# Kernel tuning notes

Measured on AMD Instinct MI355X. Metric: run time of the kernel, lower is better.

## Reference

```python
import jax, jax.numpy as jnp
import numpy as np
from jax import lax

LEVEL = 128  # level_num

def _bn(x, g, b, m, v):
    # inference-mode BatchNorm, channel axis = 1
    sh = (1, -1) + (1,) * (x.ndim - 2)
    return (x - m.reshape(sh)) * (g.reshape(sh) * lax.rsqrt(v.reshape(sh) + 1e-5)) + b.reshape(sh)

def _leaky(a):
    return jnp.where(a > 0, a, 0.01 * a)

def _l2n(a):
    return a / jnp.maximum(jnp.linalg.norm(a, axis=1, keepdims=True), 1e-12)

def _resize_bilinear_ac(x, oh, ow):
    # bilinear, align_corners=True, NCHW
    n, c, h, w = x.shape
    ys = jnp.linspace(0.0, h - 1.0, oh)
    xs = jnp.linspace(0.0, w - 1.0, ow)
    y0 = jnp.floor(ys).astype(jnp.int32)
    x0 = jnp.floor(xs).astype(jnp.int32)
    y1 = jnp.minimum(y0 + 1, h - 1)
    x1 = jnp.minimum(x0 + 1, w - 1)
    wy = (ys - y0)[:, None]
    wx = (xs - x0)[None, :]
    Y0, Y1, X0, X1 = y0[:, None], y1[:, None], x0[None, :], x1[None, :]
    return (x[:, :, Y0, X0] * (1 - wy) * (1 - wx) + x[:, :, Y0, X1] * (1 - wy) * wx
            + x[:, :, Y1, X0] * wy * (1 - wx) + x[:, :, Y1, X1] * wy * wx)

def _forward(x, conv1_w, bn1_g, bn1_b, bn1_m, bn1_v, conv2_w, f1_w, f2_w, f2_g, f2_b, f2_m, f2_v,
             out1_w, out1_g, out1_b, out1_m, out1_v, k_w, q_w, v_w, out_w, out_g, out_b, out_m, out_v):
    # conv1: 3x3 conv + BN + LeakyReLU
    y = lax.conv_general_dilated(x, conv1_w, (1, 1), 'SAME', dimension_numbers=('NCHW', 'OIHW', 'NCHW'))
    y = _leaky(_bn(y, bn1_g, bn1_b, bn1_m, bn1_v))
    # conv2: 1x1 conv, 256->128
    x2 = jnp.einsum('nchw,oc->nohw', y, conv2_w)
    N, C, H, W = x2.shape  # C = 128
    x_ave = x2.mean(axis=(2, 3), keepdims=True)  # [N,C,1,1]
    cos = (_l2n(x_ave) * _l2n(x2)).sum(1)        # [N,H,W]
    sh, sw = H // 3, W // 3
    L = sh * sw
    # H,W divisible by 3 -> adaptive_avg_pool2d is identity
    cs = cos.reshape(N, 3, sh, 3, sw).transpose(0, 1, 3, 2, 4).reshape(N, 9, L).transpose(0, 2, 1)  # [N,L,9]
    # LBP bit packing vs center (index 4); weight 0 at index 4 (strict > gives 0 there)
    bits = (cs > cs[:, :, 4:5]).astype(x.dtype)
    wts = jnp.array([1, 2, 4, 8, 0, 16, 32, 64, 128], dtype=x.dtype)
    code = (bits * wts).sum(-1)  # [N,L]
    mn = code.min(-1, keepdims=True)
    mx = code.max(-1, keepdims=True)
    code = (code - mn) / (mx - mn)
    cmin = code.min(-1, keepdims=True)
    cmax = code.max(-1, keepdims=True)
    qlv = (2 * jnp.arange(LEVEL, dtype=x.dtype) + 1) / (2 * LEVEL) * (cmax - cmin) + cmin  # [N,LEVEL]
    inter = (qlv[:, 1] - qlv[:, 0])[:, None, None]  # [N,1,1]
    quant = 1 - jnp.abs(qlv[:, None, :] - code[:, :, None])  # [N,L,LEVEL]
    quant = jnp.where(quant > 1 - inter, quant, 0.0)
    sta = quant.sum(1)                                       # [N,LEVEL]
    sta = sta / sta.sum(-1, keepdims=True)
    sta2 = jnp.stack([qlv, sta], axis=1)                     # [N,2,LEVEL]
    h1 = _leaky(jnp.einsum('ncl,oc->nol', sta2, f1_w))       # f1: 2->64
    h2 = jax.nn.relu(_bn(jnp.einsum('ncl,oc->nol', h1, f2_w), f2_g, f2_b, f2_m, f2_v))  # f2: 64->128
    xa = jnp.broadcast_to(x_ave[:, :, 0, 0][:, :, None], (N, C, LEVEL))
    s = jnp.concatenate([h2, xa], axis=1)                    # [N,256,LEVEL]
    s = jax.nn.relu(_bn(jnp.einsum('ncl,oc->nol', s, out1_w), out1_g, out1_b, out1_m, out1_v))
    k = jnp.einsum('ncl,oc->nol', s, k_w)
    q = jnp.einsum('ncl,oc->nol', s, q_w)
    v = jnp.einsum('ncl,oc->nol', s, v_w)
    w = jax.nn.softmax(jnp.einsum('ncl,ncm->nlm', k, q), axis=-1)  # bmm(k^T, q)
    f = jnp.einsum('nlm,ncm->ncl', w, v)                            # bmm(w, v^T) then transpose
    f = jax.nn.relu(_bn(jnp.einsum('ncl,oc->nol', f, out_w), out_g, out_b, out_m, out_v))
    out = jnp.einsum('ncl,npl->ncp', f, quant).reshape(N, 256, sh, sh)  # bmm(f, quant^T)
    return _resize_bilinear_ac(out, H, W)

def setup_inputs() -> dict:
    key = jax.random.key(0)
    ks = jax.random.split(key, 16)
    f32 = jnp.float32
    def nrm(k, shape, s=0.05):
        return s * jax.random.normal(k, shape, f32)
    def bnp(k, c):
        k1, k2, k3, k4 = jax.random.split(k, 4)
        return (1.0 + 0.1 * jax.random.normal(k1, (c,), f32),
                0.1 * jax.random.normal(k2, (c,), f32),
                0.1 * jax.random.normal(k3, (c,), f32),
                jax.random.uniform(k4, (c,), f32, 0.5, 1.5))
    d = {}
    d['x'] = jax.random.normal(ks[0], (32, 512, 48, 48), f32)
    d['conv1_w'] = nrm(ks[1], (256, 512, 3, 3))
    d['bn1_g'], d['bn1_b'], d['bn1_m'], d['bn1_v'] = bnp(ks[2], 256)
    d['conv2_w'] = nrm(ks[3], (128, 256))
    d['f1_w'] = nrm(ks[4], (64, 2), 0.3)
    d['f2_w'] = nrm(ks[5], (128, 64), 0.1)
    d['f2_g'], d['f2_b'], d['f2_m'], d['f2_v'] = bnp(ks[6], 128)
    d['out1_w'] = nrm(ks[7], (256, 256))
    d['out1_g'], d['out1_b'], d['out1_m'], d['out1_v'] = bnp(ks[8], 256)
    d['k_w'] = nrm(ks[9], (256, 256))
    d['q_w'] = nrm(ks[10], (256, 256))
    d['v_w'] = nrm(ks[11], (256, 256))
    d['out_w'] = nrm(ks[12], (256, 256))
    d['out_g'], d['out_b'], d['out_m'], d['out_v'] = bnp(ks[13], 256)
    return d

def reference(x, conv1_w, bn1_g, bn1_b, bn1_m, bn1_v, conv2_w, f1_w, f2_w, f2_g, f2_b, f2_m, f2_v,
              out1_w, out1_g, out1_b, out1_m, out1_v, k_w, q_w, v_w, out_w, out_g, out_b, out_m, out_v):
    return _forward(x, conv1_w, bn1_g, bn1_b, bn1_m, bn1_v, conv2_w, f1_w, f2_w, f2_g, f2_b, f2_m, f2_v,
                    out1_w, out1_g, out1_b, out1_m, out1_v, k_w, q_w, v_w, out_w, out_g, out_b, out_m, out_v)
```

## Files before the change

### kernel.cpp

```cpp
#include <hip/hip_runtime.h>
#include <math.h>

#define N_IMG 32
#define P2304 2304
#define CIN 512
#define CMID 256
#define C2 128
#define LEV 128

typedef _Float16 half8 __attribute__((ext_vector_type(8)));
typedef float f32x16 __attribute__((ext_vector_type(16)));
typedef unsigned short u16;
typedef unsigned int u32;

__device__ __forceinline__ float wredSum(float v){
#pragma unroll
  for (int o = 32; o > 0; o >>= 1) v += __shfl_down(v, o, 64);
  return v;
}
__device__ __forceinline__ float wredMax(float v){
#pragma unroll
  for (int o = 32; o > 0; o >>= 1) v = fmaxf(v, __shfl_down(v, o, 64));
  return v;
}
__device__ __forceinline__ float wredMin(float v){
#pragma unroll
  for (int o = 32; o > 0; o >>= 1) v = fminf(v, __shfl_down(v, o, 64));
  return v;
}

__device__ __forceinline__ void gll16(const void* g, void* l){
  __builtin_amdgcn_global_load_lds(
      (const __attribute__((address_space(1))) void*)g,
      (__attribute__((address_space(3))) void*)l, 16, 0, 0);
}

__global__ void prep_w1_kernel(const float* __restrict__ w1,
                               uint4* __restrict__ Wh, uint4* __restrict__ Wl){
  int fid = blockIdx.x * 256 + threadIdx.x;
  int lam = fid & 63;
  int c32 = (fid >> 6) & 3;
  int cot = (fid >> 8) & 1;
  int kt  = fid >> 9;
  int co = cot * 128 + c32 * 32 + (lam & 31);
  half8 vh, vl;
#pragma unroll
  for (int j = 0; j < 8; ++j){
    int k = kt * 16 + ((lam >> 5) << 3) + j;
    int r = k >> 9;
    int ci = k & 511;
    float v = w1[co * (CIN * 9) + ci * 9 + r];
    _Float16 h = (_Float16)v;
    vh[j] = h;
    vl[j] = (_Float16)((v - (float)h) * 2048.0f);
  }
  Wh[fid] = *(uint4*)&vh;
  Wl[fid] = *(uint4*)&vl;
}

__global__ void prep_w2_kernel(const float* __restrict__ w2,
                               uint4* __restrict__ Wh, uint4* __restrict__ Wl){
  int fid = blockIdx.x * 256 + threadIdx.x;
  int lam = fid & 63;
  int c32 = (fid >> 6) & 3;
  int kt  = fid >> 8;
  int co = c32 * 32 + (lam & 31);
  half8 vh, vl;
#pragma unroll
  for (int j = 0; j < 8; ++j){
    int k = kt * 16 + ((lam >> 5) << 3) + j;
    float v = w2[co * CMID + k];
    _Float16 h = (_Float16)v;
    vh[j] = h;
    vl[j] = (_Float16)((v - (float)h) * 2048.0f);
  }
  Wh[fid] = *(uint4*)&vh;
  Wl[fid] = *(uint4*)&vl;
}

__global__ void prep_bn_kernel(const float* __restrict__ g1, const float* __restrict__ b1,
                               const float* __restrict__ m1, const float* __restrict__ v1,
                               float* __restrict__ s1, float* __restrict__ t1){
  int c = threadIdx.x;
  float s = g1[c] * (1.0f / sqrtf(v1[c] + 1e-5f));
  s1[c] = s;
  t1[c] = b1[c] - m1[c] * s;
}

__global__ void prep_x_kernel(const float* __restrict__ x,
                              u16* __restrict__ xh, u16* __restrict__ xl,
                              int n0){
  __shared__ float tile[128 * 49];
  const int t = threadIdx.x;
  const int b = blockIdx.x;
  const int n_loc = b / 50;
  const int hp = b - n_loc * 50;
  const int n = n0 + n_loc;
  const int h = hp - 1;
  const bool vrow = (h >= 0) && (h < 48);
  const size_t base_n = (size_t)n_loc * 1280000;
  for (int cc = 0; cc < 4; ++cc){
    if (vrow){
      const float* src = x + (((size_t)n * 512 + cc * 128) * 48 + h) * 48;
#pragma unroll
      for (int i = 0; i < 24; ++i){
        int idx = t + 256 * i;
        int w = idx % 48;
        int c = idx / 48;
        tile[c * 49 + w] = src[(size_t)c * 2304 + w];
      }
    }
    __syncthreads();
    for (int i = 0; i < 13; ++i){
      int idx = t + 256 * i;
      if (idx < 3200){
        int ck_loc = idx / 400;
        int rem = idx - ck_loc * 400;
        int wp = rem >> 3;
        int clp = rem & 7;
        int w = wp - 1;
        int c_loc = ck_loc * 16 + clp * 2;
        float v0 = 0.f, v1 = 0.f;
        if (vrow && (unsigned)w < 48u){
          v0 = tile[c_loc * 49 + w];
          v1 = tile[(c_loc + 1) * 49 + w];
        }
        _Float16 h0 = (_Float16)v0, h1 = (_Float16)v1;
        _Float16 l0 = (_Float16)((v0 - (float)h0) * 2048.0f);
        _Float16 l1 = (_Float16)((v1 - (float)h1) * 2048.0f);
        union { _Float16 hh[2]; u32 uu; } ph, pl;
        ph.hh[0] = h0; ph.hh[1] = h1;
        pl.hh[0] = l0; pl.hh[1] = l1;
        size_t off = base_n + ((size_t)(cc * 8 + ck_loc) * 2500
                               + hp * 50 + wp) * 16 + clp * 2;
        *(u32*)(xh + off) = ph.uu;
        *(u32*)(xl + off) = pl.uu;
      }
    }
    __syncthreads();
  }
}

#define COMPUTE_M(CUR, KF)                                                    \
  {                                                                           \
    const int ct0 = (g & 1) * 2, pt0 = (g >> 1) * 2;                          \
    half8 fAh[2], fAl[2], fBh[2], fBl[2];                                     \
    _Pragma("unroll")                                                         \
    for (int a = 0; a < 2; ++a){                                              \
      fAh[a] = *(half8*)&Abuf[CUR][KF][0][(ct0 + a) * 512 + lam * 8];         \
      fAl[a] = *(half8*)&Abuf[CUR][KF][1][(ct0 + a) * 512 + lam * 8];         \
      fBh[a] = *(half8*)&Bbuf[CUR][KF][0][(pt0 + a) * 512 + lam * 8];         \
      fBl[a] = *(half8*)&Bbuf[CUR][KF][1][(pt0 + a) * 512 + lam * 8];         \
    }                                                                         \
    _Pragma("unroll")                                                         \
    for (int a = 0; a < 2; ++a)                                               \
      _Pragma("unroll")                                                       \
      for (int b = 0; b < 2; ++b){                                            \
        acc_hh[a][b] = __builtin_amdgcn_mfma_f32_32x32x16_f16(                \
            fAh[a], fBh[b], acc_hh[a][b], 0, 0, 0);                           \
        acc_x[a][b] = __builtin_amdgcn_mfma_f32_32x32x16_f16(                 \
            fAh[a], fBl[b], acc_x[a][b], 0, 0, 0);                            \
        acc_x[a][b] = __builtin_amdgcn_mfma_f32_32x32x16_f16(                 \
            fAl[a], fBh[b], acc_x[a][b], 0, 0, 0);                            \
      }                                                                       \
  }

#define WAITV8  asm volatile("s_waitcnt vmcnt(8)"  ::: "memory")
#define WAITV0  asm volatile("s_waitcnt vmcnt(0)"  ::: "memory")
#define BARSB { __builtin_amdgcn_s_barrier(); __builtin_amdgcn_sched_barrier(0); }

template<int NC>
__global__ __launch_bounds__(256, 2) void conv1_lds_kernel(
    const u16* __restrict__ xh, const u16* __restrict__ xl,
    const uint4* __restrict__ Wh, const uint4* __restrict__ Wl,
    const float* __restrict__ s1, const float* __restrict__ t1,
    u16* __restrict__ yh, u16* __restrict__ yl, int n0)
{
  __shared__ _Float16 Abuf[2][2][2][2048];
  __shared__ _Float16 Bbuf[2][2][2][2048];
  const int t = threadIdx.x;
  const int lam = t & 63;
  const int g = t >> 6;

  const int xcd = blockIdx.x & 7;
  const int rest = blockIdx.x >> 3;
  const int NPX = NC / 8;
  const int n_loc = xcd * NPX + rest / 36;
  const int inner = rest % 36;
  const int pt_blk = inner % 18;
  const int cot = inner / 18;
  const int n = n0 + n_loc;

  const int pbase = pt_blk * 128;
  const int khi = lam >> 5;
  const int pp = (g << 5) + (lam & 31);
  const int p = pbase + pp;
  const int ph = p / 48, pw = p - ph * 48;
  const u16* xh_n = xh + (size_t)n_loc * 1280000;
  const u16* xl_n = xl + (size_t)n_loc * 1280000;

  const int S = 144;

  f32x16 acc_hh[2][2], acc_x[2][2];
#pragma unroll
  for (int a = 0; a < 2; ++a)
#pragma unroll
    for (int b = 0; b < 2; ++b){
#pragma unroll
      for (int e = 0; e < 16; ++e){ acc_hh[a][b][e] = 0.f; acc_x[a][b][e] = 0.f; }
    }

#define ISSUE1(SV, BUF)                                                       \
  {                                                                           \
    int s_ = (SV);                                                            \
    int k0_ = 2 * s_;                                                         \
    _Pragma("unroll")                                                         \
    for (int kf = 0; kf < 2; ++kf){                                           \
      int fg_ = ((k0_ + kf) * 2 + cot) * 4 + g;                               \
      gll16(Wh + fg_ * 64 + lam, &Abuf[BUF][kf][0][t * 8]);                   \
      gll16(Wl + fg_ * 64 + lam, &Abuf[BUF][kf][1][t * 8]);                   \
    }                                                                         \
    int r_ = k0_ >> 5;                                          \
    int ck0_ = k0_ & 31;                         \
    int qpp_ = (ph + r_ / 3) * 50 + (pw + r_ % 3);            \
    _Pragma("unroll")                                                         \
    for (int kf = 0; kf < 2; ++kf){                                           \
      size_t o_ = ((size_t)(ck0_ + kf) * 2500 + qpp_) * 16 + (khi << 3);      \
      gll16(xh_n + o_, &Bbuf[BUF][kf][0][t * 8]);                             \
      gll16(xl_n + o_, &Bbuf[BUF][kf][1][t * 8]);                             \
    }                                                                         \
  }

  ISSUE1(0, 0);
  ISSUE1(1, 1);

  for (int s = 0; s < S - 1; ++s){
    WAITV8;
    BARSB;
    __builtin_amdgcn_s_setprio(1);
    COMPUTE_M(s & 1, 0);
    COMPUTE_M(s & 1, 1);
    __builtin_amdgcn_s_setprio(0);
    if (s + 2 < S){
      BARSB;
      ISSUE1(s + 2, s & 1);
    }
  }
  WAITV0;
  BARSB;
  __builtin_amdgcn_s_setprio(1);
  COMPUTE_M((S - 1) & 1, 0);
  COMPUTE_M((S - 1) & 1, 1);
  __builtin_amdgcn_s_setprio(0);
#undef ISSUE1

  const int cobase = cot * 128;
#pragma unroll
  for (int a = 0; a < 2; ++a){
    const int ctile = (g & 1) * 2 + a;
#pragma unroll
    for (int b = 0; b < 2; ++b){
      const int ptile = (g >> 1) * 2 + b;
      const int pg = pbase + ptile * 32 + (lam & 31);
#pragma unroll
      for (int q = 0; q < 4; ++q){
        const int co0 = cobase + ctile * 32 + 8 * q + 4 * khi;
        const int co16 = co0 >> 4, col = co0 & 15;
        union { _Float16 h[4]; uint2 u; } Uh, Ul;
#pragma unroll
        for (int i = 0; i < 4; ++i){
          const int rg = 4 * q + i;
          const int co = co0 + i;
          float val = acc_hh[a][b][rg] + acc_x[a][b][rg] * (1.0f / 2048.0f);
          val = val * s1[co] + t1[co];
          val = val > 0.f ? val : 0.01f * val;
          _Float16 h = (_Float16)val;
          Uh.h[i] = h;
          Ul.h[i] = (_Float16)((val - (float)h) * 2048.0f);
        }
        size_t off = (((size_t)n * 16 + co16) * P2304 + pg) * 16 + col;
        *(uint2*)(yh + off) = Uh.u;
        *(uint2*)(yl + off) = Ul.u;
      }
    }
  }
}

__global__ __launch_bounds__(256, 2) void conv2_lds_kernel(
    const u16* __restrict__ yh, const u16* __restrict__ yl,
    const uint4* __restrict__ Wh, const uint4* __restrict__ Wl,
    float* __restrict__ out)
{
  __shared__ _Float16 Abuf[2][2][2][2048];
  __shared__ _Float16 Bbuf[2][2][2][2048];
  const int t = threadIdx.x;
  const int lam = t & 63;
  const int g = t >> 6;

  const int pt_blk = blockIdx.x % 18;
  const int n = blockIdx.x / 18;
  const int pbase = pt_blk * 128;
  const int khi = lam >> 5;
  const int p = pbase + (g << 5) + (lam & 31);
  const u16* yh_n = yh + (size_t)n * 589824;
  const u16* yl_n = yl + (size_t)n * 589824;

  const int S = 8;

  f32x16 acc_hh[2][2], acc_x[2][2];
#pragma unroll
  for (int a = 0; a < 2; ++a)
#pragma unroll
    for (int b = 0; b < 2; ++b){
#pragma unroll
      for (int e = 0; e < 16; ++e){ acc_hh[a][b][e] = 0.f; acc_x[a][b][e] = 0.f; }
    }

#define ISSUE2(SV, BUF)                                                       \
  {                                                                           \
    int s_ = (SV);                                                            \
    int k0_ = 2 * s_;                                                         \
    _Pragma("unroll")                                                         \
    for (int kf = 0; kf < 2; ++kf){                                           \
      int fg_ = (k0_ + kf) * 4 + g;                                           \
      gll16(Wh + fg_ * 64 + lam, &Abuf[BUF][kf][0][t * 8]);                   \
      gll16(Wl + fg_ * 64 + lam, &Abuf[BUF][kf][1][t * 8]);                   \
    }                                                                         \
    _Pragma("unroll")                                                         \
    for (int kf = 0; kf < 2; ++kf){                                           \
      size_t o_ = ((size_t)(k0_ + kf) * P2304 + p) * 16 + (khi << 3);         \
      gll16(yh_n + o_, &Bbuf[BUF][kf][0][t * 8]);                             \
      gll16(yl_n + o_, &Bbuf[BUF][kf][1][t * 8]);                             \
    }                                                                         \
  }

  ISSUE2(0, 0);
  ISSUE2(1, 1);

  for (int s = 0; s < S - 1; ++s){
    WAITV8;
    BARSB;
    __builtin_amdgcn_s_setprio(1);
    COMPUTE_M(s & 1, 0);
    COMPUTE_M(s & 1, 1);
    __builtin_amdgcn_s_setprio(0);
    if (s + 2 < S){
      BARSB;
      ISSUE2(s + 2, s & 1);
    }
  }
  WAITV0;
  BARSB;
  __builtin_amdgcn_s_setprio(1);
  COMPUTE_M((S - 1) & 1, 0);
  COMPUTE_M((S - 1) & 1, 1);
  __builtin_amdgcn_s_setprio(0);
#undef ISSUE2

#pragma unroll
  for (int a = 0; a < 2; ++a){
    const int ctile = (g & 1) * 2 + a;
#pragma unroll
    for (int b = 0; b < 2; ++b){
      const int ptile = (g >> 1) * 2 + b;
      const int pg = pbase + ptile * 32 + (lam & 31);
#pragma unroll
      for (int rg = 0; rg < 16; ++rg){
        const int row = (rg & 3) + 8 * (rg >> 2) + 4 * khi;
        const int co = ctile * 32 + row;
        float val = acc_hh[a][b][rg] + acc_x[a][b][rg] * (1.0f / 2048.0f);
        out[((size_t)n * C2 + co) * P2304 + pg] = val;
      }
    }
  }
}

template<int R, int CPT, int COTN, bool BN>
__global__ __launch_bounds__(256, 2) void conv_mfma_kernel(
    const float* __restrict__ in, const uint4* __restrict__ Wh, const uint4* __restrict__ Wl,
    const float* __restrict__ s1, const float* __restrict__ t1, float* __restrict__ out)
{
  __shared__ _Float16 Abuf[2][2][2][2048];
  __shared__ _Float16 Bbuf[2][2][2][2048];
  const int t = threadIdx.x;
  const int lam = t & 63;
  const int g = t >> 6;

  int n, pt_blk, cot;
  if (COTN == 2){
    int xcd = blockIdx.x & 7;
    int rest = blockIdx.x >> 3;
    n = xcd * 4 + rest / 36;
    int inner = rest % 36;
    pt_blk = inner % 18;
    cot = inner / 18;
  } else {
    pt_blk = blockIdx.x % 18;
    cot = 0;
    n = blockIdx.x / 18;
  }
  const int pbase = pt_blk * 128;
  const int cobase = cot * 128;

  const int khi = lam >> 5;
  const int pp = (g << 5) + (lam & 31);
  const int p = pbase + pp;
  const int ph = p / 48, pw = p - ph * 48;
  const float* in_n = in + (size_t)n * CPT * P2304;

  const int S = (R * CPT) / 32;
  const int KTPT = CPT / 16;

  f32x16 acc_hh[2][2], acc_x[2][2];
#pragma unroll
  for (int a = 0; a < 2; ++a)
#pragma unroll
    for (int b = 0; b < 2; ++b){
#pragma unroll
      for (int e = 0; e < 16; ++e){ acc_hh[a][b][e] = 0.f; acc_x[a][b][e] = 0.f; }
    }

  uint4 rAh[2], rAl[2];
  float rB[16];
  bool vmask;

#define ISSUE(SV)                                                             \
  {                                                                           \
    int s_ = (SV);                                                            \
    _Pragma("unroll")                                                         \
    for (int kf = 0; kf < 2; ++kf){                                           \
      int fi = (((2 * s_ + kf) * COTN + cot) * 4 + g) * 64 + lam;             \
      rAh[kf] = Wh[fi];                                                       \
      rAl[kf] = Wl[fi];                                                       \
    }                                                                         \
    int r_ = (R == 1) ? 0 : ((2 * s_) / KTPT);                                \
    int cbase_ = ((2 * s_) % KTPT) * 16;                                      \
    int dh_ = (R == 1) ? 0 : (r_ / 3 - 1);                                    \
    int dw_ = (R == 1) ? 0 : (r_ - (r_ / 3) * 3 - 1);                         \
    int hh_ = ph + dh_, ww_ = pw + dw_;                                       \
    vmask = ((unsigned)hh_ < 48u) & ((unsigned)ww_ < 48u);                    \
    int hc_ = min(max(hh_, 0), 47), wc_ = min(max(ww_, 0), 47);               \
    const float* src_ = in_n + hc_ * 48 + wc_                                 \
                        + (size_t)(cbase_ + khi * 8) * P2304;                 \
    _Pragma("unroll")                                                         \
    for (int kf = 0; kf < 2; ++kf)                                            \
      _Pragma("unroll")                                                       \
      for (int j = 0; j < 8; ++j)                                             \
        rB[kf * 8 + j] = src_[(kf * 16 + j) * P2304];                         \
  }

#define STASH(NXT)                                                            \
  {                                                                           \
    _Pragma("unroll")                                                         \
    for (int kf = 0; kf < 2; ++kf){                                           \
      *(uint4*)&Abuf[NXT][kf][0][t * 8] = rAh[kf];                            \
      *(uint4*)&Abuf[NXT][kf][1][t * 8] = rAl[kf];                            \
      half8 vh, vl;                                                           \
      _Pragma("unroll")                                                       \
      for (int j = 0; j < 8; ++j){                                            \
        float v = vmask ? rB[kf * 8 + j] : 0.0f;                              \
        _Float16 h = (_Float16)v;                                             \
        vh[j] = h;                                                            \
        vl[j] = (_Float16)((v - (float)h) * 2048.0f);                         \
      }                                                                       \
      *(half8*)&Bbuf[NXT][kf][0][t * 8] = vh;                                 \
      *(half8*)&Bbuf[NXT][kf][1][t * 8] = vl;                                 \
    }                                                                         \
  }

  ISSUE(0);
  STASH(0);
  __syncthreads();

  for (int s = 0; s < S; ++s){
    const int cur = s & 1, nxt = cur ^ 1;
    const bool more = (s + 1 < S);
    if (more) ISSUE(s + 1);
    COMPUTE_M(cur, 0);
    if (more) STASH(nxt);
    COMPUTE_M(cur, 1);
    __syncthreads();
  }
#undef ISSUE
#undef STASH

  const int M = COTN * 128;
#pragma unroll
  for (int a = 0; a < 2; ++a){
    const int ctile = (g & 1) * 2 + a;
#pragma unroll
    for (int b = 0; b < 2; ++b){
      const int ptile = (g >> 1) * 2 + b;
      const int pg = pbase + ptile * 32 + (lam & 31);
#pragma unroll
      for (int rg = 0; rg < 16; ++rg){
        const int row = (rg & 3) + 8 * (rg >> 2) + 4 * (lam >> 5);
        const int co = cobase + ctile * 32 + row;
        float val = acc_hh[a][b][rg] + acc_x[a][b][rg] * (1.0f / 2048.0f);
        if (BN){
          val = val * s1[co] + t1[co];
          val = val > 0.f ? val : 0.01f * val;
        }
        out[((size_t)n * M + co) * P2304 + pg] = val;
      }
    }
  }
}

__global__ void xave_kernel(const float* __restrict__ x2, float* __restrict__ xave){
  __shared__ float red[4];
  int nc = blockIdx.x, t = threadIdx.x;
  const float* row = x2 + nc * P2304;
  float s = 0.f;
#pragma unroll
  for (int i = 0; i < 9; i++) s += row[t + 256 * i];
  float w = wredSum(s);
  if ((t & 63) == 0) red[t >> 6] = w;
  __syncthreads();
  if (t == 0) xave[nc] = (red[0] + red[1] + red[2] + red[3]) * (1.0f / 2304.0f);
}

__global__ void xan_kernel(const float* __restrict__ xave, float* __restrict__ xan){
  __shared__ float red[2];
  int n = blockIdx.x, t = threadIdx.x;
  float v = xave[n * 128 + t];
  float w = wredSum(v * v);
  if ((t & 63) == 0) red[t >> 6] = w;
  __syncthreads();
  float norm = fmaxf(sqrtf(red[0] + red[1]), 1e-12f);
  xan[n * 128 + t] = v / norm;
}

__global__ void cos_kernel(const float* __restrict__ x2, const float* __restrict__ xan,
                           float* __restrict__ cosb){
  int idx = blockIdx.x * 256 + threadIdx.x;
  if (idx >= N_IMG * P2304) return;
  int n = idx / P2304;
  int p = idx - n * P2304;
  const float* xp = x2 + n * C2 * P2304 + p;
  const float* an = xan + n * 128;
  float dot = 0.f, ss = 0.f;
  for (int c = 0; c < 128; c++){
    float v = xp[c * P2304];
    dot += an[c] * v;
    ss  += v * v;
  }
  cosb[idx] = dot / fmaxf(sqrtf(ss), 1e-12f);
}

__global__ void lbp_kernel(const float* __restrict__ cosb, float* __restrict__ code,
                           float* __restrict__ qlv){
  __shared__ float red[4];
  int n = blockIdx.x;
  int l = threadIdx.x;
  int ir = l >> 4, ic = l & 15;
  const float* cn = cosb + n * P2304;
  float cs4 = cn[(16 + ir) * 48 + (16 + ic)];
  const float wts[9] = {1.f, 2.f, 4.f, 8.f, 0.f, 16.f, 32.f, 64.f, 128.f};
  float codev = 0.f;
#pragma unroll
  for (int j = 0; j < 9; j++){
    int jr = j / 3, jc = j - 3 * (j / 3);
    float vv = cn[(jr * 16 + ir) * 48 + (jc * 16 + ic)];
    if (vv > cs4) codev += wts[j];
  }
  float w;
  w = wredMin(codev);
  if ((l & 63) == 0) red[l >> 6] = w;
  __syncthreads();
  float mn = fminf(fminf(red[0], red[1]), fminf(red[2], red[3]));
  __syncthreads();
  w = wredMax(codev);
  if ((l & 63) == 0) red[l >> 6] = w;
  __syncthreads();
  float mx = fmaxf(fmaxf(red[0], red[1]), fmaxf(red[2], red[3]));
  __syncthreads();
  float cd = (codev - mn) / (mx - mn);
  w = wredMin(cd);
  if ((l & 63) == 0) red[l >> 6] = w;
  __syncthreads();
  float cmin = fminf(fminf(red[0], red[1]), fminf(red[2], red[3]));
  __syncthreads();
  w = wredMax(cd);
  if ((l & 63) == 0) red[l >> 6] = w;
  __syncthreads();
  float cmax = fmaxf(fmaxf(red[0], red[1]), fmaxf(red[2], red[3]));
  code[n * 256 + l] = cd;
  if (l < 128){
    float tmp = (float)(2 * l + 1) * (1.0f / 256.0f);
    qlv[n * 128 + l] = tmp * (cmax - cmin) + cmin;
  }
}

__global__ void quant_kernel(const float* __restrict__ code, const float* __restrict__ qlv,
                             float* __restrict__ quantT){
  __shared__ float cs[256];
  __shared__ float qs[128];
  int n = blockIdx.x, t = threadIdx.x;
  cs[t] = code[n * 256 + t];
  if (t < 128) qs[t] = qlv[n * 128 + t];
  __syncthreads();
  float thr = 1.0f - (qs[1] - qs[0]);
  float* dst = quantT + n * LEV * 256;
#pragma unroll 4
  for (int i = 0; i < 128; i++){
    int v = t + 256 * i;
    int lv = v >> 8;
    int p = v & 255;
    float qq = 1.0f - fabsf(qs[lv] - cs[p]);
    dst[v] = (qq > thr) ? qq : 0.f;
  }
}

__global__ void sta_rows_kernel(const float* __restrict__ quantT, float* __restrict__ raw){
  int b = blockIdx.x;
  int t = threadIdx.x;
  int n = b >> 5;
  int row = (b & 31) * 4 + (t >> 6);
  int lane = t & 63;
  const float* src = quantT + ((size_t)(n * LEV + row)) * 256 + lane * 4;
  float4 v = *(const float4*)src;
  float s = v.x + v.y + v.z + v.w;
  s = wredSum(s);
  if (lane == 0) raw[n * 128 + row] = s;
}

__global__ void sta_norm_kernel(const float* __restrict__ raw, float* __restrict__ sta){
  __shared__ float red[2];
  int n = blockIdx.x, t = threadIdx.x;
  float v = raw[n * 128 + t];
  float w = wredSum(v);
  if ((t & 63) == 0) red[t >> 6] = w;
  __syncthreads();
  sta[n * 128 + t] = v / (red[0] + red[1]);
}

__global__ void h2_fused_kernel(const float* __restrict__ f1w, const float* __restrict__ f2w,
                                const float* __restrict__ qlv, const float* __restrict__ sta,
                                const float* __restrict__ g, const float* __restrict__ bb,
                                const float* __restrict__ mm, const float* __restrict__ vv,
                                float* __restrict__ h2){
  int idx = blockIdx.x * 256 + threadIdx.x;
  if (idx >= N_IMG * 32 * 128) return;
  int l = idx & 127;
  int o0 = ((idx >> 7) & 31) << 2;
  int n = idx >> 12;
  float qv = qlv[n * 128 + l];
  float sv = sta[n * 128 + l];
  const float* w0 = f2w + (o0 + 0) * 64;
  const float* w1 = f2w + (o0 + 1) * 64;
  const float* w2 = f2w + (o0 + 2) * 64;
  const float* w3 = f2w + (o0 + 3) * 64;
  float a0 = 0, a1 = 0, a2 = 0, a3 = 0;
  for (int c = 0; c < 64; c++){
    float hv = f1w[2 * c] * qv + f1w[2 * c + 1] * sv;
    hv = hv > 0.f ? hv : 0.01f * hv;
    a0 += w0[c] * hv; a1 += w1[c] * hv; a2 += w2[c] * hv; a3 += w3[c] * hv;
  }
  float av[4] = {a0, a1, a2, a3};
#pragma unroll
  for (int j = 0; j < 4; j++){
    int o = o0 + j;
    float s = g[o] * (1.0f / sqrtf(vv[o] + 1e-5f));
    float val = (av[j] - mm[o]) * s + bb[o];
    h2[(n * 128 + o) * 128 + l] = fmaxf(val, 0.f);
  }
}

__global__ void out1_fused_kernel(const float* __restrict__ Wm, const float* __restrict__ h2,
                                  const float* __restrict__ xave,
                                  const float* __restrict__ g, const float* __restrict__ bb,
                                  const float* __restrict__ mm, const float* __restrict__ vv,
                                  float* __restrict__ s2){
  int idx = blockIdx.x * 256 + threadIdx.x;
  if (idx >= N_IMG * 64 * 128) return;
  int l = idx & 127;
  int o0 = ((idx >> 7) & 63) << 2;
  int n = idx >> 13;
  const float* h2n = h2 + (n * 128) * 128 + l;
  const float* xa = xave + n * 128;
  const float* w0 = Wm + (o0 + 0) * 256;
  const float* w1 = Wm + (o0 + 1) * 256;
  const float* w2 = Wm + (o0 + 2) * 256;
  const float* w3 = Wm + (o0 + 3) * 256;
  float a0 = 0, a1 = 0, a2 = 0, a3 = 0;
  for (int c = 0; c < 128; c++){
    float bv = h2n[c * 128];
    a0 += w0[c] * bv; a1 += w1[c] * bv; a2 += w2[c] * bv; a3 += w3[c] * bv;
  }
  for (int c = 0; c < 128; c++){
    float bv = xa[c];
    a0 += w0[128 + c] * bv; a1 += w1[128 + c] * bv;
    a2 += w2[128 + c] * bv; a3 += w3[128 + c] * bv;
  }
  float av[4] = {a0, a1, a2, a3};
#pragma unroll
  for (int j = 0; j < 4; j++){
    int o = o0 + j;
    float s = g[o] * (1.0f / sqrtf(vv[o] + 1e-5f));
    float val = (av[j] - mm[o]) * s + bb[o];
    s2[(n * 256 + o) * 128 + l] = fmaxf(val, 0.f);
  }
}

__global__ void gemm_w_kernel(const float* __restrict__ Wm, const float* __restrict__ B,
                              float* __restrict__ Cout, int Cdim, int O, int total, int mode,
                              const float* __restrict__ g, const float* __restrict__ bb,
                              const float* __restrict__ mm, const float* __restrict__ vv){
  int idx = blockIdx.x * 256 + threadIdx.x;
  if (idx >= total) return;
  int per_n = (O >> 2) << 7;
  int n = idx / per_n;
  int rem = idx - n * per_n;
  int o0 = (rem >> 7) << 2;
  int l = rem & 127;
  const float* Bn = B + (n * Cdim) * 128 + l;
  const float* w0 = Wm + (o0 + 0) * Cdim;
  const float* w1 = Wm + (o0 + 1) * Cdim;
  const float* w2 = Wm + (o0 + 2) * Cdim;
  const float* w3 = Wm + (o0 + 3) * Cdim;
  float a0 = 0, a1 = 0, a2 = 0, a3 = 0;
  for (int c = 0; c < Cdim; c++){
    float bv = Bn[c * 128];
    a0 += w0[c] * bv; a1 += w1[c] * bv; a2 += w2[c] * bv; a3 += w3[c] * bv;
  }
  float av[4] = {a0, a1, a2, a3};
#pragma unroll
  for (int j = 0; j < 4; j++){
    int o = o0 + j;
    float val = av[j];
    if (mode == 1){
      float s = g[o] * (1.0f / sqrtf(vv[o] + 1e-5f));
      val = (val - mm[o]) * s + bb[o];
      val = fmaxf(val, 0.f);
    }
    Cout[(n * O + o) * 128 + l] = val;
  }
}

__global__ void gemm_kqv_kernel(const float* __restrict__ kW, const float* __restrict__ qW,
                                const float* __restrict__ vW, const float* __restrict__ B,
                                float* __restrict__ kO, float* __restrict__ qO,
                                float* __restrict__ vO){
  int idx = blockIdx.x * 256 + threadIdx.x;
  int sel = idx >> 18;
  int rem = idx & 262143;
  const float* Wm = (sel == 0) ? kW : (sel == 1) ? qW : vW;
  float* Cout     = (sel == 0) ? kO : (sel == 1) ? qO : vO;
  int n = rem >> 13;
  int r2 = rem & 8191;
  int o0 = (r2 >> 7) << 2;
  int l = r2 & 127;
  const float* Bn = B + (n * 256) * 128 + l;
  const float* w0 = Wm + (o0 + 0) * 256;
  const float* w1 = Wm + (o0 + 1) * 256;
  const float* w2 = Wm + (o0 + 2) * 256;
  const float* w3 = Wm + (o0 + 3) * 256;
  float a0 = 0, a1 = 0, a2 = 0, a3 = 0;
  for (int c = 0; c < 256; c++){
    float bv = Bn[c * 128];
    a0 += w0[c] * bv; a1 += w1[c] * bv; a2 += w2[c] * bv; a3 += w3[c] * bv;
  }
  float* dst = Cout + (n * 256 + o0) * 128 + l;
  dst[0] = a0; dst[128] = a1; dst[256] = a2; dst[384] = a3;
}

__global__ void attn_scsm_kernel(const float* __restrict__ k, const float* __restrict__ q,
                                 float* __restrict__ scT){
  __shared__ float redm[2][2][4];
  __shared__ float reds[2][2][4];
  int b = blockIdx.x;
  int t = threadIdx.x;
  int n = b >> 4;
  int h = t >> 7;
  int wv = (t >> 6) & 1;
  int lane = t & 63;
  int m = t & 127;
  int l0 = (((b & 15) * 2 + h)) * 4;
  const float* kn = k + n * 256 * 128;
  const float* qn = q + n * 256 * 128 + m;
  float a0 = 0, a1 = 0, a2 = 0, a3 = 0;
  for (int c = 0; c < 256; c++){
    float qv = qn[c * 128];
    const float* kr = kn + c * 128 + l0;
    a0 += kr[0] * qv; a1 += kr[1] * qv; a2 += kr[2] * qv; a3 += kr[3] * qv;
  }
  float av[4] = {a0, a1, a2, a3};
#pragma unroll
  for (int r = 0; r < 4; r++){
    float w = wredMax(av[r]);
    if (lane == 0) redm[h][wv][r] = w;
  }
  __syncthreads();
  float ex[4];
#pragma unroll
  for (int r = 0; r < 4; r++){
    float mx = fmaxf(redm[h][0][r], redm[h][1][r]);
    ex[r] = expf(av[r] - mx);
    float s = wredSum(ex[r]);
    if (lane == 0) reds[h][wv][r] = s;
  }
  __syncthreads();
  float* dst = scT + n * 16384 + m * 128 + l0;
#pragma unroll
  for (int r = 0; r < 4; r++){
    dst[r] = ex[r] / (reds[h][0][r] + reds[h][1][r]);
  }
}

__global__ void attn_f_kernel(const float* __restrict__ vb, const float* __restrict__ scT,
                              float* __restrict__ f){
  int idx = blockIdx.x * 256 + threadIdx.x;
  if (idx >= N_IMG * 64 * 128) return;
  int l = idx & 127;
  int c0 = ((idx >> 7) & 63) << 2;
  int n = idx >> 13;
  const float* vn = vb + (n * 256 + c0) * 128;
  const float* sn = scT + n * 128 * 128 + l;
  float a0 = 0, a1 = 0, a2 = 0, a3 = 0;
  for (int m = 0; m < 128; m++){
    float sv = sn[m * 128];
    a0 += vn[m] * sv; a1 += vn[128 + m] * sv; a2 += vn[256 + m] * sv; a3 += vn[384 + m] * sv;
  }
  float* dst = f + (n * 256 + c0) * 128 + l;
  dst[0] = a0; dst[128] = a1; dst[256] = a2; dst[384] = a3;
}

__global__ void final_kernel(const float* __restrict__ g, const float* __restrict__ quantT,
                             float* __restrict__ outs){
  int idx = blockIdx.x * 256 + threadIdx.x;
  if (idx >= N_IMG * 64 * 256) return;
  int p = idx & 255;
  int c0 = ((idx >> 8) & 63) << 2;
  int n = idx >> 14;
  const float* gn = g + (n * 256 + c0) * 128;
  const float* qn = quantT + (n * LEV) * 256 + p;
  float a0 = 0, a1 = 0, a2 = 0, a3 = 0;
  for (int lv = 0; lv < 128; lv++){
    float qv = qn[lv * 256];
    a0 += gn[lv] * qv; a1 += gn[128 + lv] * qv; a2 += gn[256 + lv] * qv; a3 += gn[384 + lv] * qv;
  }
  float* dst = outs + (n * 256 + c0) * 256 + p;
  dst[0] = a0; dst[256] = a1; dst[512] = a2; dst[768] = a3;
}

__global__ void resize_kernel(const float* __restrict__ outs, float* __restrict__ dout){
  int idx = blockIdx.x * 256 + threadIdx.x;
  if (idx >= N_IMG * 256 * P2304) return;
  int ow = idx % 48;
  int tmp = idx / 48;
  int oh = tmp % 48;
  int nc = tmp / 48;
  const float* src = outs + nc * 256;
  float fy = oh * (15.0f / 47.0f);
  float fx = ow * (15.0f / 47.0f);
  int y0 = (int)fy;
  int x0 = (int)fx;
  int y1 = min(y0 + 1, 15);
  int x1 = min(x0 + 1, 15);
  float wy = fy - (float)y0;
  float wx = fx - (float)x0;
  float v00 = src[y0 * 16 + x0], v01 = src[y0 * 16 + x1];
  float v10 = src[y1 * 16 + x0], v11 = src[y1 * 16 + x1];
  dout[idx] = v00 * (1.f - wy) * (1.f - wx) + v01 * (1.f - wy) * wx
            + v10 * wy * (1.f - wx) + v11 * wy * wx;
}

extern "C" void kernel_launch(void* const* d_in, const int* in_sizes, int n_in,
                              void* d_out, int out_size, void* d_ws, size_t ws_size,
                              hipStream_t stream)
{
  const float* x       = (const float*)d_in[0];
  const float* conv1_w = (const float*)d_in[1];
  const float* bn1_g   = (const float*)d_in[2];
  const float* bn1_b   = (const float*)d_in[3];
  const float* bn1_m   = (const float*)d_in[4];
  const float* bn1_v   = (const float*)d_in[5];
  const float* conv2_w = (const float*)d_in[6];
  const float* f1_w    = (const float*)d_in[7];
  const float* f2_w    = (const float*)d_in[8];
  const float* f2_g    = (const float*)d_in[9];
  const float* f2_b    = (const float*)d_in[10];
  const float* f2_m    = (const float*)d_in[11];
  const float* f2_v    = (const float*)d_in[12];
  const float* out1_w  = (const float*)d_in[13];
  const float* out1_g  = (const float*)d_in[14];
  const float* out1_b  = (const float*)d_in[15];
  const float* out1_m  = (const float*)d_in[16];
  const float* out1_v  = (const float*)d_in[17];
  const float* k_w     = (const float*)d_in[18];
  const float* q_w     = (const float*)d_in[19];
  const float* v_w     = (const float*)d_in[20];
  const float* out_w   = (const float*)d_in[21];
  const float* out_g   = (const float*)d_in[22];
  const float* out_b   = (const float*)d_in[23];
  const float* out_m   = (const float*)d_in[24];
  const float* out_v   = (const float*)d_in[25];

  float* ws = (float*)d_ws;
  float* dout = (float*)d_out;

  float* w_y   = ws;
  float* w_x2  = ws + 18874368;
  float* w_W1h = ws + 28311552;
  float* w_W1l = ws + 28901376;
  float* w_W2h = ws + 29491200;
  float* w_W2l = ws + 29507584;
  float* w_s1  = ws + 29523968;
  float* w_t1  = ws + 29524224;
  float* w_xave = w_y + 0;
  float* w_xan  = w_y + 4096;
  float* w_cos  = w_y + 8192;
  float* w_code = w_y + 81920;
  float* w_qlv  = w_y + 90112;
  float* w_sta  = w_y + 94208;
  float* w_quant= w_y + 98304;
  float* w_h2   = w_y + 1409024;
  float* w_k    = w_y + 2981888;
  float* w_q    = w_y + 4030464;
  float* w_v    = w_y + 5079040;
  float* w_scT  = w_y + 6651904;
  float* w_f    = w_y + 7176192;
  float* w_g    = w_y + 8224768;
  float* w_outs = w_y + 9273344;
  float* w_s2   = w_y + 11370496;
  float* w_raw  = w_y + 12419072;

  prep_w1_kernel<<<576, 256, 0, stream>>>(conv1_w, (uint4*)w_W1h, (uint4*)w_W1l);
  prep_w2_kernel<<<16, 256, 0, stream>>>(conv2_w, (uint4*)w_W2h, (uint4*)w_W2l);
  prep_bn_kernel<<<1, 256, 0, stream>>>(bn1_g, bn1_b, bn1_m, bn1_v, w_s1, w_t1);

  const size_t BASE_F = 29524480;
  const size_t XPI_F  = 640000;
  const size_t ws_f = ws_size / 4;
  int NCc = 0;
  if (ws_f >= BASE_F + 2 * 32 * XPI_F)      NCc = 32;
  else if (ws_f >= BASE_F + 2 * 16 * XPI_F) NCc = 16;

  if (NCc > 0){
    u16* w_xh = (u16*)(ws + BASE_F);
    u16* w_xl = w_xh + (size_t)NCc * 1280000;
    u16* w_yh = (u16*)w_y;
    u16* w_yl = (u16*)(w_y + 9437184);
    const int nchunk = N_IMG / NCc;
    for (int c = 0; c < nchunk; ++c){
      int n0 = c * NCc;
      prep_x_kernel<<<NCc * 50, 256, 0, stream>>>(x, w_xh, w_xl, n0);
      if (NCc == 32)
        conv1_lds_kernel<32><<<1152, 256, 0, stream>>>(
            w_xh, w_xl, (const uint4*)w_W1h, (const uint4*)w_W1l, w_s1, w_t1,
            w_yh, w_yl, n0);
      else
        conv1_lds_kernel<16><<<576, 256, 0, stream>>>(
            w_xh, w_xl, (const uint4*)w_W1h, (const uint4*)w_W1l, w_s1, w_t1,
            w_yh, w_yl, n0);
    }
    conv2_lds_kernel<<<576, 256, 0, stream>>>(
        w_yh, w_yl, (const uint4*)w_W2h, (const uint4*)w_W2l, w_x2);
  } else {
    conv_mfma_kernel<9, 512, 2, true><<<1152, 256, 0, stream>>>(
        x, (const uint4*)w_W1h, (const uint4*)w_W1l, w_s1, w_t1, w_y);
    conv_mfma_kernel<1, 256, 1, false><<<576, 256, 0, stream>>>(
        w_y, (const uint4*)w_W2h, (const uint4*)w_W2l, w_s1, w_t1, w_x2);
  }

  xave_kernel<<<4096, 256, 0, stream>>>(w_x2, w_xave);
  xan_kernel<<<32, 128, 0, stream>>>(w_xave, w_xan);
  cos_kernel<<<288, 256, 0, stream>>>(w_x2, w_xan, w_cos);
  lbp_kernel<<<32, 256, 0, stream>>>(w_cos, w_code, w_qlv);
  quant_kernel<<<32, 256, 0, stream>>>(w_code, w_qlv, w_quant);
  sta_rows_kernel<<<1024, 256, 0, stream>>>(w_quant, w_raw);
  sta_norm_kernel<<<32, 128, 0, stream>>>(w_raw, w_sta);
  h2_fused_kernel<<<512, 256, 0, stream>>>(f1_w, f2_w, w_qlv, w_sta,
                                           f2_g, f2_b, f2_m, f2_v, w_h2);
  out1_fused_kernel<<<1024, 256, 0, stream>>>(out1_w, w_h2, w_xave,
                                              out1_g, out1_b, out1_m, out1_v, w_s2);
  gemm_kqv_kernel<<<3072, 256, 0, stream>>>(k_w, q_w, v_w, w_s2, w_k, w_q, w_v);
  attn_scsm_kernel<<<512, 256, 0, stream>>>(w_k, w_q, w_scT);
  attn_f_kernel<<<1024, 256, 0, stream>>>(w_v, w_scT, w_f);
  gemm_w_kernel<<<1024, 256, 0, stream>>>(out_w, w_f, w_g, 256, 256, N_IMG * 64 * 128, 1,
                                          out_g, out_b, out_m, out_v);
  final_kernel<<<2048, 256, 0, stream>>>(w_g, w_quant, w_outs);
  resize_kernel<<<73728, 256, 0, stream>>>(w_outs, dout);
}
```

Baseline: 1.485 ms.

## Fuse LBP, quantization and statistics kernels; stage conv1 weights in LDS for prep

```diff
diff --git a/kernel.cpp b/kernel.cpp
--- a/kernel.cpp
+++ b/kernel.cpp
@@ -37,25 +37,29 @@
 
 __global__ void prep_w1_kernel(const float* __restrict__ w1,
                                uint4* __restrict__ Wh, uint4* __restrict__ Wl){
-  int fid = blockIdx.x * 256 + threadIdx.x;
-  int lam = fid & 63;
-  int c32 = (fid >> 6) & 3;
-  int cot = (fid >> 8) & 1;
-  int kt  = fid >> 9;
-  int co = cot * 128 + c32 * 32 + (lam & 31);
-  half8 vh, vl;
-#pragma unroll
-  for (int j = 0; j < 8; ++j){
-    int k = kt * 16 + ((lam >> 5) << 3) + j;
-    int r = k >> 9;
-    int ci = k & 511;
-    float v = w1[co * (CIN * 9) + ci * 9 + r];
-    _Float16 h = (_Float16)v;
-    vh[j] = h;
-    vl[j] = (_Float16)((v - (float)h) * 2048.0f);
-  }
-  Wh[fid] = *(uint4*)&vh;
-  Wl[fid] = *(uint4*)&vl;
+  __shared__ float wbuf[4608];
+  const int co = blockIdx.x;
+  const int t = threadIdx.x;
+  const float* src = w1 + (size_t)co * 4608;
+  for (int i = t; i < 4608; i += 256) wbuf[i] = src[i];
+  __syncthreads();
+  const int cot = co >> 7, c32 = (co >> 5) & 3, cl = co & 31;
+  for (int fh = t; fh < 576; fh += 256){
+    int kt = fh >> 1, khalf = fh & 1;
+    half8 vh, vl;
+#pragma unroll
+    for (int j = 0; j < 8; ++j){
+      int k = kt * 16 + khalf * 8 + j;
+      int r = k >> 9, ci = k & 511;
+      float v = wbuf[ci * 9 + r];
+      _Float16 h = (_Float16)v;
+      vh[j] = h;
+      vl[j] = (_Float16)((v - (float)h) * 2048.0f);
+    }
+    int fid = ((kt * 2 + cot) * 4 + c32) * 64 + khalf * 32 + cl;
+    Wh[fid] = *(uint4*)&vh;
+    Wl[fid] = *(uint4*)&vl;
+  }
 }
 
 __global__ void prep_w2_kernel(const float* __restrict__ w2,
@@ -548,12 +552,18 @@
   cosb[idx] = dot / fmaxf(sqrtf(ss), 1e-12f);
 }
 
-__global__ void lbp_kernel(const float* __restrict__ cosb, float* __restrict__ code,
-                           float* __restrict__ qlv){
+__global__ void lbp_quant_sta_kernel(const float* __restrict__ cosb,
+                                     float* __restrict__ qlv,
+                                     float* __restrict__ quantT,
+                                     float* __restrict__ sta){
   __shared__ float red[4];
+  __shared__ float cs[256];
+  __shared__ float qs[128];
+  __shared__ float rsw[4][128];
   int n = blockIdx.x;
   int l = threadIdx.x;
   int ir = l >> 4, ic = l & 15;
+  int wv = l >> 6, lane = l & 63;
   const float* cn = cosb + n * P2304;
   float cs4 = cn[(16 + ir) * 48 + (16 + ic)];
   const float wts[9] = {1.f, 2.f, 4.f, 8.f, 0.f, 16.f, 32.f, 64.f, 128.f};
@@ -566,73 +576,52 @@
   }
   float w;
   w = wredMin(codev);
-  if ((l & 63) == 0) red[l >> 6] = w;
+  if (lane == 0) red[wv] = w;
   __syncthreads();
   float mn = fminf(fminf(red[0], red[1]), fminf(red[2], red[3]));
   __syncthreads();
   w = wredMax(codev);
-  if ((l & 63) == 0) red[l >> 6] = w;
+  if (lane == 0) red[wv] = w;
   __syncthreads();
   float mx = fmaxf(fmaxf(red[0], red[1]), fmaxf(red[2], red[3]));
   __syncthreads();
   float cd = (codev - mn) / (mx - mn);
   w = wredMin(cd);
-  if ((l & 63) == 0) red[l >> 6] = w;
+  if (lane == 0) red[wv] = w;
   __syncthreads();
   float cmin = fminf(fminf(red[0], red[1]), fminf(red[2], red[3]));
   __syncthreads();
   w = wredMax(cd);
-  if ((l & 63) == 0) red[l >> 6] = w;
+  if (lane == 0) red[wv] = w;
   __syncthreads();
   float cmax = fmaxf(fmaxf(red[0], red[1]), fmaxf(red[2], red[3]));
-  code[n * 256 + l] = cd;
+  cs[l] = cd;
   if (l < 128){
     float tmp = (float)(2 * l + 1) * (1.0f / 256.0f);
-    qlv[n * 128 + l] = tmp * (cmax - cmin) + cmin;
-  }
-}
-
-__global__ void quant_kernel(const float* __restrict__ code, const float* __restrict__ qlv,
-                             float* __restrict__ quantT){
-  __shared__ float cs[256];
-  __shared__ float qs[128];
-  int n = blockIdx.x, t = threadIdx.x;
-  cs[t] = code[n * 256 + t];
-  if (t < 128) qs[t] = qlv[n * 128 + t];
+    float qv = tmp * (cmax - cmin) + cmin;
+    qs[l] = qv;
+    qlv[n * 128 + l] = qv;
+  }
   __syncthreads();
   float thr = 1.0f - (qs[1] - qs[0]);
+  float myc = cs[l];
   float* dst = quantT + n * LEV * 256;
-#pragma unroll 4
   for (int i = 0; i < 128; i++){
-    int v = t + 256 * i;
-    int lv = v >> 8;
-    int p = v & 255;
-    float qq = 1.0f - fabsf(qs[lv] - cs[p]);
-    dst[v] = (qq > thr) ? qq : 0.f;
-  }
-}
-
-__global__ void sta_rows_kernel(const float* __restrict__ quantT, float* __restrict__ raw){
-  int b = blockIdx.x;
-  int t = threadIdx.x;
-  int n = b >> 5;
-  int row = (b & 31) * 4 + (t >> 6);
-  int lane = t & 63;
-  const float* src = quantT + ((size_t)(n * LEV + row)) * 256 + lane * 4;
-  float4 v = *(const float4*)src;
-  float s = v.x + v.y + v.z + v.w;
-  s = wredSum(s);
-  if (lane == 0) raw[n * 128 + row] = s;
-}
-
-__global__ void sta_norm_kernel(const float* __restrict__ raw, float* __restrict__ sta){
-  __shared__ float red[2];
-  int n = blockIdx.x, t = threadIdx.x;
-  float v = raw[n * 128 + t];
-  float w = wredSum(v);
-  if ((t & 63) == 0) red[t >> 6] = w;
-  __syncthreads();
-  sta[n * 128 + t] = v / (red[0] + red[1]);
+    float qq = 1.0f - fabsf(qs[i] - myc);
+    qq = (qq > thr) ? qq : 0.f;
+    dst[i * 256 + l] = qq;
+    float s = wredSum(qq);
+    if (lane == 0) rsw[wv][i] = s;
+  }
+  __syncthreads();
+  if (l < 128){
+    float rowsum = rsw[0][l] + rsw[1][l] + rsw[2][l] + rsw[3][l];
+    float tt = wredSum(rowsum);
+    if ((l & 63) == 0) red[l >> 6] = tt;
+    __syncthreads();
+    float total = red[0] + red[1];
+    sta[n * 128 + l] = rowsum / total;
+  }
 }
 
 __global__ void h2_fused_kernel(const float* __restrict__ f1w, const float* __restrict__ f2w,
@@ -911,7 +900,6 @@
   float* w_xave = w_y + 0;
   float* w_xan  = w_y + 4096;
   float* w_cos  = w_y + 8192;
-  float* w_code = w_y + 81920;
   float* w_qlv  = w_y + 90112;
   float* w_sta  = w_y + 94208;
   float* w_quant= w_y + 98304;
@@ -924,9 +912,8 @@
   float* w_g    = w_y + 8224768;
   float* w_outs = w_y + 9273344;
   float* w_s2   = w_y + 11370496;
-  float* w_raw  = w_y + 12419072;
-
-  prep_w1_kernel<<<576, 256, 0, stream>>>(conv1_w, (uint4*)w_W1h, (uint4*)w_W1l);
+
+  prep_w1_kernel<<<256, 256, 0, stream>>>(conv1_w, (uint4*)w_W1h, (uint4*)w_W1l);
   prep_w2_kernel<<<16, 256, 0, stream>>>(conv2_w, (uint4*)w_W2h, (uint4*)w_W2l);
   prep_bn_kernel<<<1, 256, 0, stream>>>(bn1_g, bn1_b, bn1_m, bn1_v, w_s1, w_t1);
 
@@ -967,10 +954,7 @@
   xave_kernel<<<4096, 256, 0, stream>>>(w_x2, w_xave);
   xan_kernel<<<32, 128, 0, stream>>>(w_xave, w_xan);
   cos_kernel<<<288, 256, 0, stream>>>(w_x2, w_xan, w_cos);
-  lbp_kernel<<<32, 256, 0, stream>>>(w_cos, w_code, w_qlv);
-  quant_kernel<<<32, 256, 0, stream>>>(w_code, w_qlv, w_quant);
-  sta_rows_kernel<<<1024, 256, 0, stream>>>(w_quant, w_raw);
-  sta_norm_kernel<<<32, 128, 0, stream>>>(w_raw, w_sta);
+  lbp_quant_sta_kernel<<<32, 256, 0, stream>>>(w_cos, w_qlv, w_quant, w_sta);
   h2_fused_kernel<<<512, 256, 0, stream>>>(f1_w, f2_w, w_qlv, w_sta,
                                            f2_g, f2_b, f2_m, f2_v, w_h2);
   out1_fused_kernel<<<1024, 256, 0, stream>>>(out1_w, w_h2, w_xave,
```

Measured after the change: 1.460 ms. About the same (-1.7%).
